# Optimization experiments

Hardware: AMD Instinct MI355X
Metric: run time of the kernel (lower is better)

The kernel has to match this reference:

```python
import jax, jax.numpy as jnp
import numpy as np

N_NODES = 100000


def gcn_conv(x, src, dst, W, b, n):
    # PyG GCNConv: add self-loops, symmetric deg^-1/2 normalization,
    # linear transform, gather->scatter-add aggregation, + bias.
    loop = jnp.arange(n, dtype=src.dtype)
    s = jnp.concatenate([src, loop])
    d = jnp.concatenate([dst, loop])
    deg = jax.ops.segment_sum(jnp.ones_like(d, dtype=x.dtype), d, num_segments=n)
    dinv = jnp.where(deg > 0, jax.lax.rsqrt(deg), jnp.zeros_like(deg))
    norm = dinv[s] * dinv[d]            # [E+N]
    h = x @ W                            # [N, out] (transform before propagate)
    msg = h[s] * norm[:, None]           # gather + scale
    out = jax.ops.segment_sum(msg, d, num_segments=n)  # scatter-add to dst
    return out + b


def setup_inputs() -> dict:
    key = jax.random.key(0)
    k = jax.random.split(key, 6)
    n, e, c_in, hid, c_out = N_NODES, 2500000, 5, 32, 1
    x = jax.random.normal(k[0], (n, c_in), dtype=jnp.float32)
    edge_index = jax.random.randint(k[1], (2, e), 0, n, dtype=jnp.int64)
    # Glorot-style init for GCN weights, zero bias (PyG default)
    W1 = jax.random.normal(k[2], (c_in, hid), dtype=jnp.float32) * (1.0 / np.sqrt(c_in))
    b1 = jnp.zeros((hid,), dtype=jnp.float32)
    W2 = jax.random.normal(k[3], (hid, c_out), dtype=jnp.float32) * (1.0 / np.sqrt(hid))
    b2 = jnp.zeros((c_out,), dtype=jnp.float32)
    return {"x": x, "edge_index": edge_index, "W1": W1, "b1": b1, "W2": W2, "b2": b2}


def reference(x, edge_index, W1, b1, W2, b2):
    n = x.shape[0]
    src, dst = edge_index[0], edge_index[1]
    h = jax.nn.relu(gcn_conv(x, src, dst, W1, b1, n))
    # dropout p=0.3 is identity at inference (training=False)
    return jax.nn.sigmoid(gcn_conv(h, src, dst, W2, b2, n))
```

## Files before the change

kernel.cpp:

```cpp
#include <hip/hip_runtime.h>
#include <math.h>


#define NB_SHIFT  8
#define BNODES    256
#define NBK       512
#define CAP       8192
#define CAP_SHIFT 13
#define CHUNK     4888
#define PBLK      512
#define RPT0      3
#define RPT4      4
#define GBS       16

struct SMemP0 {
    int sp[CHUNK];
    unsigned short sb[CHUNK];
    int cnt[NBK], ofs[NBK], cur[NBK], gbase[NBK];
    int wtmp[8];
};
struct SMemP1 {
    int stage2[CAP];
    int ofs[BNODES], cnt[BNODES], cur[BNODES];
    float w1[160], bb1[32], w2[32];
    int wtmp[8];
};
union SMem { SMemP0 p0; SMemP1 p1; };

__device__ __forceinline__ void gbar_arrive(int* bar, int blk, int tid) {
    __syncthreads();
    if (tid == 0) {
        __threadfence();
        __hip_atomic_fetch_add(&bar[(blk & 7) * GBS], 1, __ATOMIC_RELAXED,
                               __HIP_MEMORY_SCOPE_AGENT);
    }
}
__device__ __forceinline__ void gbar_wait(int* bar, int tgt, int tid) {
    if (tid == 0) {
        for (;;) {
            int s = 0;
#pragma unroll
            for (int k = 0; k < 8; ++k)
                s += __hip_atomic_load(&bar[k * GBS], __ATOMIC_RELAXED,
                                       __HIP_MEMORY_SCOPE_AGENT);
            if (s >= tgt) break;
            __builtin_amdgcn_s_sleep(1);
        }
        __threadfence();
    }
    __syncthreads();
}

__global__ __launch_bounds__(PBLK, 4) void k_fused(
        const int* __restrict__ src, const int* __restrict__ dst, int E,
        const float* __restrict__ x,
        const float* __restrict__ W1, const float* __restrict__ b1,
        const float* __restrict__ W2, const float* __restrict__ b2,
        float* __restrict__ out,
        int* __restrict__ pairs, int* __restrict__ bcur, int* __restrict__ gbar,
        float* __restrict__ h2s, float* __restrict__ xs, int n, int nb) {
    __shared__ SMem sm;
    const int tid  = threadIdx.x;
    const int blk  = blockIdx.x;
    const int G    = gridDim.x;
    const int lane = tid & 63, wv = tid >> 6;
    const int nbase = blk << NB_SHIFT;

    {
        int base = blk * CHUNK;
        if (base < E) {
            int m = min(CHUNK, E - base);
            int m4 = m >> 2;
            int4 dv[RPT0], sv[RPT0];
            int nv = 0;
            const int4* d4 = (const int4*)(dst + base);
            const int4* s4g = (const int4*)(src + base);
#pragma unroll
            for (int j = 0; j < RPT0; ++j) {
                int idx = tid + j * PBLK;
                if (idx < m4) { dv[j] = d4[idx]; sv[j] = s4g[idx]; nv = j + 1; }
            }
            int tb = (m4 << 2) + tid;
            int td = 0, ts = 0, tvalid = 0;
            if (tb < m) { td = dst[base + tb]; ts = src[base + tb]; tvalid = 1; }
            sm.p0.cnt[tid] = 0;
            __syncthreads();
#pragma unroll
            for (int j = 0; j < RPT0; ++j) if (j < nv) {
                atomicAdd(&sm.p0.cnt[dv[j].x >> NB_SHIFT], 1);
                atomicAdd(&sm.p0.cnt[dv[j].y >> NB_SHIFT], 1);
                atomicAdd(&sm.p0.cnt[dv[j].z >> NB_SHIFT], 1);
                atomicAdd(&sm.p0.cnt[dv[j].w >> NB_SHIFT], 1);
            }
            if (tvalid) atomicAdd(&sm.p0.cnt[td >> NB_SHIFT], 1);
            __syncthreads();
            int v = sm.p0.cnt[tid];
            int s = v;
#pragma unroll
            for (int d = 1; d < 64; d <<= 1) {
                int t = __shfl_up(s, d);
                if (lane >= d) s += t;
            }
            if (lane == 63) sm.p0.wtmp[wv] = s;
            __syncthreads();
            if (wv == 0) {
                int t = (lane < 8) ? sm.p0.wtmp[lane] : 0;
#pragma unroll
                for (int d = 1; d < 8; d <<= 1) {
                    int u = __shfl_up(t, d);
                    if (lane >= d) t += u;
                }
                if (lane < 8) sm.p0.wtmp[lane] = t;
            }
            __syncthreads();
            int pre = s + (wv ? sm.p0.wtmp[wv - 1] : 0) - v;
            sm.p0.ofs[tid] = pre;
            sm.p0.cur[tid] = pre;
            sm.p0.gbase[tid] = (tid << CAP_SHIFT)
                             + (v ? atomicAdd(&bcur[tid], v) : 0);
            __syncthreads();
#pragma unroll
            for (int j = 0; j < RPT0; ++j) if (j < nv) {
                int b, p;
                b = dv[j].x >> NB_SHIFT; p = atomicAdd(&sm.p0.cur[b], 1);
                sm.p0.sp[p] = ((dv[j].x & (BNODES - 1)) << 24) | sv[j].x;
                sm.p0.sb[p] = (unsigned short)b;
                b = dv[j].y >> NB_SHIFT; p = atomicAdd(&sm.p0.cur[b], 1);
                sm.p0.sp[p] = ((dv[j].y & (BNODES - 1)) << 24) | sv[j].y;
                sm.p0.sb[p] = (unsigned short)b;
                b = dv[j].z >> NB_SHIFT; p = atomicAdd(&sm.p0.cur[b], 1);
                sm.p0.sp[p] = ((dv[j].z & (BNODES - 1)) << 24) | sv[j].z;
                sm.p0.sb[p] = (unsigned short)b;
                b = dv[j].w >> NB_SHIFT; p = atomicAdd(&sm.p0.cur[b], 1);
                sm.p0.sp[p] = ((dv[j].w & (BNODES - 1)) << 24) | sv[j].w;
                sm.p0.sb[p] = (unsigned short)b;
            }
            if (tvalid) {
                int b = td >> NB_SHIFT;
                int p = atomicAdd(&sm.p0.cur[b], 1);
                sm.p0.sp[p] = ((td & (BNODES - 1)) << 24) | ts;
                sm.p0.sb[p] = (unsigned short)b;
            }
            __syncthreads();
            for (int i = tid; i < m; i += PBLK) {
                int b = sm.p0.sb[i];
                pairs[sm.p0.gbase[b] + (i - sm.p0.ofs[b])] = sm.p0.sp[i];
            }
        }
    }
    gbar_arrive(gbar, blk, tid);
    float xr0 = 0.f, xr1 = 0.f, xr2 = 0.f, xr3 = 0.f, xr4 = 0.f;
    if (blk < nb) {
        if (tid < 160) sm.p1.w1[tid] = W1[tid];
        else if (tid < 192) sm.p1.bb1[tid - 160] = b1[tid - 160];
        else if (tid < 224) sm.p1.w2[tid - 192] = W2[tid - 192];
        if (tid < BNODES) {
            sm.p1.cnt[tid] = 0;
            int node = nbase + tid;
            if (node < n) {
                const float* xp = x + (size_t)node * 5;
                xr0 = xp[0]; xr1 = xp[1]; xr2 = xp[2]; xr3 = xp[3]; xr4 = xp[4];
            }
        }
    }
    gbar_wait(gbar, G, tid);

    int4 rc[RPT4];
    int nv4 = 0, rt = 0, rtv = 0;
    if (blk < nb) {
        int base = blk << CAP_SHIFT;
        int len = min(((volatile int*)bcur)[blk], CAP);
        int len4 = len >> 2;
        const int4* p4 = (const int4*)(pairs + base);
#pragma unroll
        for (int j = 0; j < RPT4; ++j) {
            int idx = tid + j * PBLK;
            if (idx < len4) { rc[j] = p4[idx]; nv4 = j + 1; }
        }
        int i = (len4 << 2) + tid;
        if (i < len) { rt = pairs[base + i]; rtv = 1; }
#pragma unroll
        for (int j = 0; j < RPT4; ++j) if (j < nv4) {
            atomicAdd(&sm.p1.cnt[((unsigned)rc[j].x) >> 24], 1);
            atomicAdd(&sm.p1.cnt[((unsigned)rc[j].y) >> 24], 1);
            atomicAdd(&sm.p1.cnt[((unsigned)rc[j].z) >> 24], 1);
            atomicAdd(&sm.p1.cnt[((unsigned)rc[j].w) >> 24], 1);
        }
        if (rtv) atomicAdd(&sm.p1.cnt[((unsigned)rt) >> 24], 1);
        __syncthreads();
        int v = (tid < BNODES) ? sm.p1.cnt[tid] : 0;
        int s = v;
#pragma unroll
        for (int d = 1; d < 64; d <<= 1) {
            int t = __shfl_up(s, d);
            if (lane >= d) s += t;
        }
        if (lane == 63 && wv < 4) sm.p1.wtmp[wv] = s;
        __syncthreads();
        if (wv == 0) {
            int t = (lane < 4) ? sm.p1.wtmp[lane] : 0;
#pragma unroll
            for (int d = 1; d < 4; d <<= 1) {
                int u = __shfl_up(t, d);
                if (lane >= d) t += u;
            }
            if (lane < 4) sm.p1.wtmp[lane] = t;
        }
        __syncthreads();
        if (tid < BNODES) {
            int pre = s + (wv ? sm.p1.wtmp[wv - 1] : 0) - v;
            sm.p1.ofs[tid] = pre;
            sm.p1.cur[tid] = pre;
            int node = nbase + tid;
            if (node < n) {
                float di = rsqrtf((float)v + 1.0f);
                float* xo = xs + ((size_t)node << 3);
                xo[0] = xr0 * di; xo[1] = xr1 * di; xo[2] = xr2 * di;
                xo[3] = xr3 * di; xo[4] = xr4 * di;
            }
        }
    }
    gbar_arrive(gbar, blk, tid);
    if (blk < nb) {
#pragma unroll
        for (int j = 0; j < RPT4; ++j) if (j < nv4) {
            int p;
            p = atomicAdd(&sm.p1.cur[((unsigned)rc[j].x) >> 24], 1);
            sm.p1.stage2[p] = rc[j].x & 0x00FFFFFF;
            p = atomicAdd(&sm.p1.cur[((unsigned)rc[j].y) >> 24], 1);
            sm.p1.stage2[p] = rc[j].y & 0x00FFFFFF;
            p = atomicAdd(&sm.p1.cur[((unsigned)rc[j].z) >> 24], 1);
            sm.p1.stage2[p] = rc[j].z & 0x00FFFFFF;
            p = atomicAdd(&sm.p1.cur[((unsigned)rc[j].w) >> 24], 1);
            sm.p1.stage2[p] = rc[j].w & 0x00FFFFFF;
        }
        if (rtv) {
            int p = atomicAdd(&sm.p1.cur[((unsigned)rt) >> 24], 1);
            sm.p1.stage2[p] = rt & 0x00FFFFFF;
        }
    }
    gbar_wait(gbar, 2 * G, tid);

    if (blk < nb) {
        int t2 = tid >> 1, half = tid & 1;
        int node = nbase + t2;
        if (node < n) {
            int beg = sm.p1.ofs[t2], dg = sm.p1.cnt[t2];
            float a0 = 0.f, a1 = 0.f, a2 = 0.f, a3 = 0.f, a4 = 0.f;
            if (!half) {
                const float* xo = xs + ((size_t)node << 3);
                a0 = xo[0]; a1 = xo[1]; a2 = xo[2]; a3 = xo[3]; a4 = xo[4];
            }
            for (int e = beg + half; e < beg + dg; e += 2) {
                int sidx = sm.p1.stage2[e];
                const float* xr = xs + ((size_t)sidx << 3);
                float4 q = *(const float4*)xr;
                float q4 = xr[4];
                a0 += q.x; a1 += q.y; a2 += q.z; a3 += q.w; a4 += q4;
            }
            a0 += __shfl_xor(a0, 1); a1 += __shfl_xor(a1, 1);
            a2 += __shfl_xor(a2, 1); a3 += __shfl_xor(a3, 1);
            a4 += __shfl_xor(a4, 1);
            if (!half) {
                float di = rsqrtf((float)dg + 1.0f);
                a0 *= di; a1 *= di; a2 *= di; a3 *= di; a4 *= di;
                float sum = 0.f;
#pragma unroll
                for (int c = 0; c < 32; ++c) {
                    float z = sm.p1.bb1[c] + a0 * sm.p1.w1[c]
                            + a1 * sm.p1.w1[32 + c] + a2 * sm.p1.w1[64 + c]
                            + a3 * sm.p1.w1[96 + c] + a4 * sm.p1.w1[128 + c];
                    sum += fmaxf(z, 0.f) * sm.p1.w2[c];
                }
                h2s[node] = sum * di;
            }
        }
    }
    gbar_arrive(gbar, blk, tid);
    gbar_wait(gbar, 3 * G, tid);

    if (blk < nb) {
        int t2 = tid >> 1, half = tid & 1;
        int node = nbase + t2;
        if (node >= n) return;
        int beg = sm.p1.ofs[t2], dg = sm.p1.cnt[t2];
        float a = 0.f;
        for (int e = beg + half; e < beg + dg; e += 2)
            a += h2s[sm.p1.stage2[e]];
        a += __shfl_xor(a, 1);
        if (!half) {
            float di = rsqrtf((float)dg + 1.0f);
            float vv = di * (a + h2s[node]) + b2[0];
            out[node] = 1.0f / (1.0f + __expf(-vv));
        }
    }
}


__global__ __launch_bounds__(512) void k_part(const int* __restrict__ src,
                                              const int* __restrict__ dst, int E,
                                              int* __restrict__ bcur,
                                              int* __restrict__ pairs) {
    __shared__ int sp[CHUNK];
    __shared__ unsigned short sb[CHUNK];
    __shared__ int cnt[NBK], ofs[NBK], cur[NBK], gbase[NBK];
    int tid = threadIdx.x;
    int base = blockIdx.x * CHUNK;
    int m = min(CHUNK, E - base);

    if (tid < NBK) cnt[tid] = 0;
    __syncthreads();
    for (int i = tid; i < m; i += 2 * 512) {
        int i1 = i + 512;
        int k0 = dst[base + i] >> NB_SHIFT;
        int k1 = (i1 < m) ? (dst[base + i1] >> NB_SHIFT) : -1;
        atomicAdd(&cnt[k0], 1);
        if (k1 >= 0) atomicAdd(&cnt[k1], 1);
    }
    __syncthreads();
    int v = cnt[tid];
    ofs[tid] = v;
    __syncthreads();
    for (int off = 1; off < NBK; off <<= 1) {
        int u = (tid >= off) ? ofs[tid - off] : 0;
        __syncthreads();
        ofs[tid] += u;
        __syncthreads();
    }
    int pre = ofs[tid] - v;
    ofs[tid] = pre;
    cur[tid] = pre;
    gbase[tid] = (tid << CAP_SHIFT) + (v ? atomicAdd(&bcur[tid], v) : 0);
    __syncthreads();
    for (int i = tid; i < m; i += 4 * 512) {
        int ia = i + 512, ib = i + 1024, ic = i + 1536;
        int s0 = src[base + i], d0 = dst[base + i];
        int s1 = 0, d1 = 0, s2 = 0, d2 = 0, s3 = 0, d3 = 0;
        if (ia < m) { s1 = src[base + ia]; d1 = dst[base + ia]; }
        if (ib < m) { s2 = src[base + ib]; d2 = dst[base + ib]; }
        if (ic < m) { s3 = src[base + ic]; d3 = dst[base + ic]; }
        int b0 = d0 >> NB_SHIFT;
        int p0 = atomicAdd(&cur[b0], 1);
        sp[p0] = ((d0 & (BNODES - 1)) << 24) | s0;
        sb[p0] = (unsigned short)b0;
        if (ia < m) {
            int b1 = d1 >> NB_SHIFT;
            int p1 = atomicAdd(&cur[b1], 1);
            sp[p1] = ((d1 & (BNODES - 1)) << 24) | s1;
            sb[p1] = (unsigned short)b1;
        }
        if (ib < m) {
            int b2 = d2 >> NB_SHIFT;
            int p2 = atomicAdd(&cur[b2], 1);
            sp[p2] = ((d2 & (BNODES - 1)) << 24) | s2;
            sb[p2] = (unsigned short)b2;
        }
        if (ic < m) {
            int b3 = d3 >> NB_SHIFT;
            int p3 = atomicAdd(&cur[b3], 1);
            sp[p3] = ((d3 & (BNODES - 1)) << 24) | s3;
            sb[p3] = (unsigned short)b3;
        }
    }
    __syncthreads();
    for (int i = tid; i < m; i += 512) {
        int b = sb[i];
        pairs[gbase[b] + (i - ofs[b])] = sp[i];
    }
}

__global__ __launch_bounds__(512) void k_sorta(const int* __restrict__ pairs,
                                               const int* __restrict__ bcur,
                                               const float* __restrict__ x,
                                               float* __restrict__ dinv,
                                               float* __restrict__ xs,
                                               int* __restrict__ nofs,
                                               int* __restrict__ deg, int n) {
    __shared__ int cnt[BNODES], scn[BNODES];
    int tid = threadIdx.x;
    int b = blockIdx.x;
    int base = b << CAP_SHIFT;
    int len = min(bcur[b], CAP);

    if (tid < BNODES) cnt[tid] = 0;
    __syncthreads();
    for (int i = tid; i < len; i += 512)
        atomicAdd(&cnt[((unsigned)pairs[base + i]) >> 24], 1);
    __syncthreads();
    int v = (tid < BNODES) ? cnt[tid] : 0;
    if (tid < BNODES) scn[tid] = v;
    __syncthreads();
    for (int off = 1; off < BNODES; off <<= 1) {
        int u = (tid < BNODES && tid >= off) ? scn[tid - off] : 0;
        __syncthreads();
        if (tid < BNODES) scn[tid] += u;
        __syncthreads();
    }
    if (tid < BNODES) {
        int node = (b << NB_SHIFT) + tid;
        if (node < n) {
            nofs[node] = base + scn[tid] - v;
            deg[node] = v;
            float di = rsqrtf((float)v + 1.0f);
            dinv[node] = di;
            const float* xr = x + (size_t)node * 5;
            float* xo = xs + ((size_t)node << 3);
#pragma unroll
            for (int k = 0; k < 5; ++k) xo[k] = xr[k] * di;
        }
    }
}

__global__ __launch_bounds__(512) void k_sortagg1(int* __restrict__ pairs,
                                                  const int* __restrict__ bcur,
                                                  const int* __restrict__ nofs,
                                                  const int* __restrict__ deg,
                                                  const float* __restrict__ xs,
                                                  const float* __restrict__ dinv,
                                                  const float* __restrict__ W1,
                                                  const float* __restrict__ b1,
                                                  const float* __restrict__ W2,
                                                  float* __restrict__ h2s, int n) {
    __shared__ int stage2[CAP];
    __shared__ int ofs[BNODES], cnt[BNODES], cur[BNODES];
    __shared__ float w1[160], bb1[32], w2[32];
    int tid = threadIdx.x;
    int b = blockIdx.x;
    int nbase = b << NB_SHIFT;
    int base = b << CAP_SHIFT;
    int len = min(bcur[b], CAP);

    if (tid < 160) w1[tid] = W1[tid];
    else if (tid < 192) bb1[tid - 160] = b1[tid - 160];
    else if (tid < 224) w2[tid - 192] = W2[tid - 192];
    if (tid < BNODES) {
        int node = nbase + tid;
        int o = 0, c = 0;
        if (node < n) { o = nofs[node] - base; c = deg[node]; }
        ofs[tid] = o; cnt[tid] = c; cur[tid] = o;
    }
    __syncthreads();
    for (int i = tid; i < len; i += 2048) {
        int ia = i + 512, ib = i + 1024, ic = i + 1536;
        int v0 = pairs[base + i];
        int v1 = (ia < len) ? pairs[base + ia] : -1;
        int v2 = (ib < len) ? pairs[base + ib] : -1;
        int v3 = (ic < len) ? pairs[base + ic] : -1;
        int p0 = atomicAdd(&cur[((unsigned)v0) >> 24], 1);
        stage2[p0] = v0 & 0x00FFFFFF;
        if (v1 != -1) {
            int p1 = atomicAdd(&cur[((unsigned)v1) >> 24], 1);
            stage2[p1] = v1 & 0x00FFFFFF;
        }
        if (v2 != -1) {
            int p2 = atomicAdd(&cur[((unsigned)v2) >> 24], 1);
            stage2[p2] = v2 & 0x00FFFFFF;
        }
        if (v3 != -1) {
            int p3 = atomicAdd(&cur[((unsigned)v3) >> 24], 1);
            stage2[p3] = v3 & 0x00FFFFFF;
        }
    }
    __syncthreads();
    {
        int len4 = len >> 2;
        const int4* s4 = (const int4*)stage2;
        int4* p4 = (int4*)(pairs + base);
        for (int i = tid; i < len4; i += 512) p4[i] = s4[i];
        for (int i = (len4 << 2) + tid; i < len; i += 512)
            pairs[base + i] = stage2[i];
    }
    int t2 = tid >> 1, half = tid & 1;
    int node = nbase + t2;
    if (node >= n) return;
    int beg = ofs[t2], dg = cnt[t2];
    float a0 = 0.f, a1 = 0.f, a2 = 0.f, a3 = 0.f, a4 = 0.f;
    if (!half) {
        const float* xo = xs + ((size_t)node << 3);
        a0 = xo[0]; a1 = xo[1]; a2 = xo[2]; a3 = xo[3]; a4 = xo[4];
    }
    for (int e = beg + half; e < beg + dg; e += 2) {
        int s = stage2[e];
        const float* xr = xs + ((size_t)s << 3);
        float4 q = *(const float4*)xr;
        float q4 = xr[4];
        a0 += q.x; a1 += q.y; a2 += q.z; a3 += q.w; a4 += q4;
    }
    a0 += __shfl_xor(a0, 1); a1 += __shfl_xor(a1, 1); a2 += __shfl_xor(a2, 1);
    a3 += __shfl_xor(a3, 1); a4 += __shfl_xor(a4, 1);
    if (half) return;
    float di = dinv[node];
    a0 *= di; a1 *= di; a2 *= di; a3 *= di; a4 *= di;
    float sum = 0.f;
#pragma unroll
    for (int c = 0; c < 32; ++c) {
        float z = bb1[c] + a0 * w1[c] + a1 * w1[32 + c] + a2 * w1[64 + c]
                         + a3 * w1[96 + c] + a4 * w1[128 + c];
        sum += fmaxf(z, 0.f) * w2[c];
    }
    h2s[node] = sum * di;
}

__global__ __launch_bounds__(256) void k_agg2(const int* __restrict__ pairs,
                                              const int* __restrict__ nofs,
                                              const int* __restrict__ deg,
                                              const float* __restrict__ h2s,
                                              const float* __restrict__ dinv,
                                              const float* __restrict__ b2,
                                              float* __restrict__ out, int n) {
    int tid = threadIdx.x;
    int node = blockIdx.x * 64 + (tid >> 2);
    int q = tid & 3;
    if (node >= n) return;
    int beg = nofs[node], dg = deg[node];
    float a = 0.f;
    for (int e = beg + q; e < beg + dg; e += 4) a += h2s[pairs[e]];
    a += __shfl_xor(a, 1);
    a += __shfl_xor(a, 2);
    if (q) return;
    float v = dinv[node] * (a + h2s[node]) + b2[0];
    out[node] = 1.0f / (1.0f + __expf(-v));
}

extern "C" void kernel_launch(void* const* d_in, const int* in_sizes, int n_in,
                              void* d_out, int out_size, void* d_ws, size_t ws_size,
                              hipStream_t stream) {
    const float* x  = (const float*)d_in[0];
    const int*   ei = (const int*)d_in[1];
    const float* W1 = (const float*)d_in[2];
    const float* b1 = (const float*)d_in[3];
    const float* W2 = (const float*)d_in[4];
    const float* b2 = (const float*)d_in[5];
    float* out = (float*)d_out;

    const int n = in_sizes[0] / 5;
    const int E = in_sizes[1] / 2;
    const int* src = ei;
    const int* dst = ei + E;
    const int nb = (n + BNODES - 1) >> NB_SHIFT;

    int* wsi = (int*)d_ws;
    int*   pairs = wsi;
    int*   bcur  = wsi + ((size_t)(nb + 1) << CAP_SHIFT);
    int*   gbar  = bcur + NBK;
    int*   deg   = gbar + 8 * GBS;
    int*   nofs  = deg + n;
    float* dinv  = (float*)(nofs + n);
    float* h2s   = dinv + n;
    float* xs    = h2s + n;

    const int nchunk = (E + CHUNK - 1) / CHUNK;
    const int g = nchunk > nb ? nchunk : nb;

    static int use_coop = -1;
    if (use_coop < 0) {
        int dev = 0, ncu = 0, maxb = 0;
        hipGetDevice(&dev);
        hipDeviceGetAttribute(&ncu, hipDeviceAttributeMultiprocessorCount, dev);
        hipError_t e = hipOccupancyMaxActiveBlocksPerMultiprocessor(
                &maxb, k_fused, PBLK, 0);
        int coop = 0;
        hipDeviceGetAttribute(&coop, hipDeviceAttributeCooperativeLaunch, dev);
        use_coop = (e == hipSuccess && coop && (long)maxb * ncu >= g) ? 1 : 0;
    }

    hipMemsetAsync(bcur, 0, (NBK + 8 * GBS) * sizeof(int), stream);

    if (use_coop) {
        void* args[] = {(void*)&src, (void*)&dst, (void*)&E, (void*)&x,
                        (void*)&W1, (void*)&b1, (void*)&W2, (void*)&b2,
                        (void*)&out, (void*)&pairs, (void*)&bcur, (void*)&gbar,
                        (void*)&h2s, (void*)&xs, (void*)&n, (void*)&nb};
        hipError_t e = hipLaunchCooperativeKernel((const void*)k_fused,
                                                  dim3(g), dim3(PBLK),
                                                  args, 0, stream);
        if (e == hipSuccess) return;
        use_coop = 0;
    }

    const int nagg = (n + 63) / 64;
    k_part<<<nchunk, 512, 0, stream>>>(src, dst, E, bcur, pairs);
    k_sorta<<<nb, 512, 0, stream>>>(pairs, bcur, x, dinv, xs, nofs, deg, n);
    k_sortagg1<<<nb, 512, 0, stream>>>(pairs, bcur, nofs, deg, xs, dinv,
                                       W1, b1, W2, h2s, n);
    k_agg2<<<nagg, 256, 0, stream>>>(pairs, nofs, deg, h2s, dinv, b2, out, n);
}
```

Baseline: 141.6 us.

## Halve node-bucket size and edge chunk to double grid in cooperative fused kernel

The cooperative fused kernel now uses 128-node buckets (1024 buckets) and edge chunks of 2444 instead of 256-node buckets and 4888-edge chunks. This roughly doubles the grid and raises occupancy to 8 blocks per CU, with four lanes per node instead of two in the aggregation phases. The aim is better latency hiding and more parallelism across CUs. In exchange the kernel makes more global atomics on bucket counters, and the larger grid adds cost to each grid barrier. If the per-bucket capacity of 4608 is exceeded, edges would be dropped.

Measured after the change: 142.0 us. About the same (+0.3%).

```diff
diff --git a/kernel.cpp b/kernel.cpp
--- a/kernel.cpp
+++ b/kernel.cpp
@@ -1,6 +1,16 @@
 #include <hip/hip_runtime.h>
 #include <math.h>
 
+
+#define PBLK      512
+#define FNB_SHIFT 7
+#define FBNODES   128
+#define FNBK      1024
+#define FCAP      4608
+#define FCHUNK    2444
+#define FRPT0     2
+#define FRPT4     3
+#define GBS       16
 
 #define NB_SHIFT  8
 #define BNODES    256
@@ -8,20 +18,17 @@
 #define CAP       8192
 #define CAP_SHIFT 13
 #define CHUNK     4888
-#define PBLK      512
-#define RPT0      3
-#define RPT4      4
-#define GBS       16
 
 struct SMemP0 {
-    int sp[CHUNK];
-    unsigned short sb[CHUNK];
-    int cnt[NBK], ofs[NBK], cur[NBK], gbase[NBK];
+    int sp[FCHUNK];
+    unsigned short sb[FCHUNK];
+    int cnt[FNBK];
+    int ofs[FNBK], cur[FNBK];
     int wtmp[8];
 };
 struct SMemP1 {
-    int stage2[CAP];
-    int ofs[BNODES], cnt[BNODES], cur[BNODES];
+    int stage2[FCAP];
+    int ofs[FBNODES], cnt[FBNODES], cur[FBNODES];
     float w1[160], bb1[32], w2[32];
     int wtmp[8];
 };
@@ -51,32 +58,32 @@
     __syncthreads();
 }
 
-__global__ __launch_bounds__(PBLK, 4) void k_fused(
+__global__ __launch_bounds__(PBLK, 8) void k_fused(
         const int* __restrict__ src, const int* __restrict__ dst, int E,
         const float* __restrict__ x,
         const float* __restrict__ W1, const float* __restrict__ b1,
         const float* __restrict__ W2, const float* __restrict__ b2,
         float* __restrict__ out,
         int* __restrict__ pairs, int* __restrict__ bcur, int* __restrict__ gbar,
-        float* __restrict__ h2s, float* __restrict__ xs, int n, int nb) {
+        float* __restrict__ h2s, float* __restrict__ xs, int n, int fnb) {
     __shared__ SMem sm;
     const int tid  = threadIdx.x;
     const int blk  = blockIdx.x;
     const int G    = gridDim.x;
     const int lane = tid & 63, wv = tid >> 6;
-    const int nbase = blk << NB_SHIFT;
+    const int nbase = blk << FNB_SHIFT;
 
     {
-        int base = blk * CHUNK;
+        int base = blk * FCHUNK;
         if (base < E) {
-            int m = min(CHUNK, E - base);
+            int m = min(FCHUNK, E - base);
             int m4 = m >> 2;
-            int4 dv[RPT0], sv[RPT0];
+            int4 dv[FRPT0], sv[FRPT0];
             int nv = 0;
-            const int4* d4 = (const int4*)(dst + base);
+            const int4* d4  = (const int4*)(dst + base);
             const int4* s4g = (const int4*)(src + base);
 #pragma unroll
-            for (int j = 0; j < RPT0; ++j) {
+            for (int j = 0; j < FRPT0; ++j) {
                 int idx = tid + j * PBLK;
                 if (idx < m4) { dv[j] = d4[idx]; sv[j] = s4g[idx]; nv = j + 1; }
             }
@@ -84,18 +91,21 @@
             int td = 0, ts = 0, tvalid = 0;
             if (tb < m) { td = dst[base + tb]; ts = src[base + tb]; tvalid = 1; }
             sm.p0.cnt[tid] = 0;
+            sm.p0.cnt[tid + PBLK] = 0;
             __syncthreads();
 #pragma unroll
-            for (int j = 0; j < RPT0; ++j) if (j < nv) {
-                atomicAdd(&sm.p0.cnt[dv[j].x >> NB_SHIFT], 1);
-                atomicAdd(&sm.p0.cnt[dv[j].y >> NB_SHIFT], 1);
-                atomicAdd(&sm.p0.cnt[dv[j].z >> NB_SHIFT], 1);
-                atomicAdd(&sm.p0.cnt[dv[j].w >> NB_SHIFT], 1);
-            }
-            if (tvalid) atomicAdd(&sm.p0.cnt[td >> NB_SHIFT], 1);
+            for (int j = 0; j < FRPT0; ++j) if (j < nv) {
+                atomicAdd(&sm.p0.cnt[dv[j].x >> FNB_SHIFT], 1);
+                atomicAdd(&sm.p0.cnt[dv[j].y >> FNB_SHIFT], 1);
+                atomicAdd(&sm.p0.cnt[dv[j].z >> FNB_SHIFT], 1);
+                atomicAdd(&sm.p0.cnt[dv[j].w >> FNB_SHIFT], 1);
+            }
+            if (tvalid) atomicAdd(&sm.p0.cnt[td >> FNB_SHIFT], 1);
             __syncthreads();
-            int v = sm.p0.cnt[tid];
-            int s = v;
+            int v0 = sm.p0.cnt[2 * tid];
+            int v1 = sm.p0.cnt[2 * tid + 1];
+            int loc = v0 + v1;
+            int s = loc;
 #pragma unroll
             for (int d = 1; d < 64; d <<= 1) {
                 int t = __shfl_up(s, d);
@@ -113,48 +123,50 @@
                 if (lane < 8) sm.p0.wtmp[lane] = t;
             }
             __syncthreads();
-            int pre = s + (wv ? sm.p0.wtmp[wv - 1] : 0) - v;
-            sm.p0.ofs[tid] = pre;
-            sm.p0.cur[tid] = pre;
-            sm.p0.gbase[tid] = (tid << CAP_SHIFT)
-                             + (v ? atomicAdd(&bcur[tid], v) : 0);
+            int pre = s - loc + (wv ? sm.p0.wtmp[wv - 1] : 0);
+            sm.p0.ofs[2 * tid] = pre;         sm.p0.cur[2 * tid] = pre;
+            sm.p0.ofs[2 * tid + 1] = pre + v0; sm.p0.cur[2 * tid + 1] = pre + v0;
+            sm.p0.cnt[2 * tid] = 2 * tid * FCAP
+                               + (v0 ? atomicAdd(&bcur[2 * tid], v0) : 0);
+            sm.p0.cnt[2 * tid + 1] = (2 * tid + 1) * FCAP
+                               + (v1 ? atomicAdd(&bcur[2 * tid + 1], v1) : 0);
             __syncthreads();
 #pragma unroll
-            for (int j = 0; j < RPT0; ++j) if (j < nv) {
+            for (int j = 0; j < FRPT0; ++j) if (j < nv) {
                 int b, p;
-                b = dv[j].x >> NB_SHIFT; p = atomicAdd(&sm.p0.cur[b], 1);
-                sm.p0.sp[p] = ((dv[j].x & (BNODES - 1)) << 24) | sv[j].x;
+                b = dv[j].x >> FNB_SHIFT; p = atomicAdd(&sm.p0.cur[b], 1);
+                sm.p0.sp[p] = ((dv[j].x & (FBNODES - 1)) << 24) | sv[j].x;
                 sm.p0.sb[p] = (unsigned short)b;
-                b = dv[j].y >> NB_SHIFT; p = atomicAdd(&sm.p0.cur[b], 1);
-                sm.p0.sp[p] = ((dv[j].y & (BNODES - 1)) << 24) | sv[j].y;
+                b = dv[j].y >> FNB_SHIFT; p = atomicAdd(&sm.p0.cur[b], 1);
+                sm.p0.sp[p] = ((dv[j].y & (FBNODES - 1)) << 24) | sv[j].y;
                 sm.p0.sb[p] = (unsigned short)b;
-                b = dv[j].z >> NB_SHIFT; p = atomicAdd(&sm.p0.cur[b], 1);
-                sm.p0.sp[p] = ((dv[j].z & (BNODES - 1)) << 24) | sv[j].z;
+                b = dv[j].z >> FNB_SHIFT; p = atomicAdd(&sm.p0.cur[b], 1);
+                sm.p0.sp[p] = ((dv[j].z & (FBNODES - 1)) << 24) | sv[j].z;
                 sm.p0.sb[p] = (unsigned short)b;
-                b = dv[j].w >> NB_SHIFT; p = atomicAdd(&sm.p0.cur[b], 1);
-                sm.p0.sp[p] = ((dv[j].w & (BNODES - 1)) << 24) | sv[j].w;
+                b = dv[j].w >> FNB_SHIFT; p = atomicAdd(&sm.p0.cur[b], 1);
+                sm.p0.sp[p] = ((dv[j].w & (FBNODES - 1)) << 24) | sv[j].w;
                 sm.p0.sb[p] = (unsigned short)b;
             }
             if (tvalid) {
-                int b = td >> NB_SHIFT;
+                int b = td >> FNB_SHIFT;
                 int p = atomicAdd(&sm.p0.cur[b], 1);
-                sm.p0.sp[p] = ((td & (BNODES - 1)) << 24) | ts;
+                sm.p0.sp[p] = ((td & (FBNODES - 1)) << 24) | ts;
                 sm.p0.sb[p] = (unsigned short)b;
             }
             __syncthreads();
             for (int i = tid; i < m; i += PBLK) {
                 int b = sm.p0.sb[i];
-                pairs[sm.p0.gbase[b] + (i - sm.p0.ofs[b])] = sm.p0.sp[i];
+                pairs[sm.p0.cnt[b] + (i - sm.p0.ofs[b])] = sm.p0.sp[i];
             }
         }
     }
     gbar_arrive(gbar, blk, tid);
     float xr0 = 0.f, xr1 = 0.f, xr2 = 0.f, xr3 = 0.f, xr4 = 0.f;
-    if (blk < nb) {
+    if (blk < fnb) {
         if (tid < 160) sm.p1.w1[tid] = W1[tid];
         else if (tid < 192) sm.p1.bb1[tid - 160] = b1[tid - 160];
         else if (tid < 224) sm.p1.w2[tid - 192] = W2[tid - 192];
-        if (tid < BNODES) {
+        if (tid < FBNODES) {
             sm.p1.cnt[tid] = 0;
             int node = nbase + tid;
             if (node < n) {
@@ -165,22 +177,22 @@
     }
     gbar_wait(gbar, G, tid);
 
-    int4 rc[RPT4];
+    int4 rc[FRPT4];
     int nv4 = 0, rt = 0, rtv = 0;
-    if (blk < nb) {
-        int base = blk << CAP_SHIFT;
-        int len = min(((volatile int*)bcur)[blk], CAP);
+    if (blk < fnb) {
+        int pbase = blk * FCAP;
+        int len = min(((volatile int*)bcur)[blk], FCAP);
         int len4 = len >> 2;
-        const int4* p4 = (const int4*)(pairs + base);
-#pragma unroll
-        for (int j = 0; j < RPT4; ++j) {
+        const int4* p4 = (const int4*)(pairs + pbase);
+#pragma unroll
+        for (int j = 0; j < FRPT4; ++j) {
             int idx = tid + j * PBLK;
             if (idx < len4) { rc[j] = p4[idx]; nv4 = j + 1; }
         }
         int i = (len4 << 2) + tid;
-        if (i < len) { rt = pairs[base + i]; rtv = 1; }
-#pragma unroll
-        for (int j = 0; j < RPT4; ++j) if (j < nv4) {
+        if (i < len) { rt = pairs[pbase + i]; rtv = 1; }
+#pragma unroll
+        for (int j = 0; j < FRPT4; ++j) if (j < nv4) {
             atomicAdd(&sm.p1.cnt[((unsigned)rc[j].x) >> 24], 1);
             atomicAdd(&sm.p1.cnt[((unsigned)rc[j].y) >> 24], 1);
             atomicAdd(&sm.p1.cnt[((unsigned)rc[j].z) >> 24], 1);
@@ -188,26 +200,23 @@
         }
         if (rtv) atomicAdd(&sm.p1.cnt[((unsigned)rt) >> 24], 1);
         __syncthreads();
-        int v = (tid < BNODES) ? sm.p1.cnt[tid] : 0;
+        int v = (tid < FBNODES) ? sm.p1.cnt[tid] : 0;
         int s = v;
 #pragma unroll
         for (int d = 1; d < 64; d <<= 1) {
             int t = __shfl_up(s, d);
             if (lane >= d) s += t;
         }
-        if (lane == 63 && wv < 4) sm.p1.wtmp[wv] = s;
+        if (lane == 63 && wv < 2) sm.p1.wtmp[wv] = s;
         __syncthreads();
         if (wv == 0) {
-            int t = (lane < 4) ? sm.p1.wtmp[lane] : 0;
-#pragma unroll
-            for (int d = 1; d < 4; d <<= 1) {
-                int u = __shfl_up(t, d);
-                if (lane >= d) t += u;
-            }
-            if (lane < 4) sm.p1.wtmp[lane] = t;
+            int t = (lane < 2) ? sm.p1.wtmp[lane] : 0;
+            int u = __shfl_up(t, 1);
+            if (lane >= 1) t += u;
+            if (lane < 2) sm.p1.wtmp[lane] = t;
         }
         __syncthreads();
-        if (tid < BNODES) {
+        if (tid < FBNODES) {
             int pre = s + (wv ? sm.p1.wtmp[wv - 1] : 0) - v;
             sm.p1.ofs[tid] = pre;
             sm.p1.cur[tid] = pre;
@@ -221,9 +230,9 @@
         }
     }
     gbar_arrive(gbar, blk, tid);
-    if (blk < nb) {
-#pragma unroll
-        for (int j = 0; j < RPT4; ++j) if (j < nv4) {
+    if (blk < fnb) {
+#pragma unroll
+        for (int j = 0; j < FRPT4; ++j) if (j < nv4) {
             int p;
             p = atomicAdd(&sm.p1.cur[((unsigned)rc[j].x) >> 24], 1);
             sm.p1.stage2[p] = rc[j].x & 0x00FFFFFF;
@@ -241,27 +250,29 @@
     }
     gbar_wait(gbar, 2 * G, tid);
 
-    if (blk < nb) {
-        int t2 = tid >> 1, half = tid & 1;
-        int node = nbase + t2;
+    if (blk < fnb) {
+        int t4 = tid >> 2, q = tid & 3;
+        int node = nbase + t4;
         if (node < n) {
-            int beg = sm.p1.ofs[t2], dg = sm.p1.cnt[t2];
+            int beg = sm.p1.ofs[t4], dg = sm.p1.cnt[t4];
             float a0 = 0.f, a1 = 0.f, a2 = 0.f, a3 = 0.f, a4 = 0.f;
-            if (!half) {
+            if (q == 0) {
                 const float* xo = xs + ((size_t)node << 3);
                 a0 = xo[0]; a1 = xo[1]; a2 = xo[2]; a3 = xo[3]; a4 = xo[4];
             }
-            for (int e = beg + half; e < beg + dg; e += 2) {
+            for (int e = beg + q; e < beg + dg; e += 4) {
                 int sidx = sm.p1.stage2[e];
                 const float* xr = xs + ((size_t)sidx << 3);
-                float4 q = *(const float4*)xr;
+                float4 qv = *(const float4*)xr;
                 float q4 = xr[4];
-                a0 += q.x; a1 += q.y; a2 += q.z; a3 += q.w; a4 += q4;
-            }
-            a0 += __shfl_xor(a0, 1); a1 += __shfl_xor(a1, 1);
-            a2 += __shfl_xor(a2, 1); a3 += __shfl_xor(a3, 1);
-            a4 += __shfl_xor(a4, 1);
-            if (!half) {
+                a0 += qv.x; a1 += qv.y; a2 += qv.z; a3 += qv.w; a4 += q4;
+            }
+            a0 += __shfl_xor(a0, 1); a0 += __shfl_xor(a0, 2);
+            a1 += __shfl_xor(a1, 1); a1 += __shfl_xor(a1, 2);
+            a2 += __shfl_xor(a2, 1); a2 += __shfl_xor(a2, 2);
+            a3 += __shfl_xor(a3, 1); a3 += __shfl_xor(a3, 2);
+            a4 += __shfl_xor(a4, 1); a4 += __shfl_xor(a4, 2);
+            if (q == 0) {
                 float di = rsqrtf((float)dg + 1.0f);
                 a0 *= di; a1 *= di; a2 *= di; a3 *= di; a4 *= di;
                 float sum = 0.f;
@@ -279,16 +290,17 @@
     gbar_arrive(gbar, blk, tid);
     gbar_wait(gbar, 3 * G, tid);
 
-    if (blk < nb) {
-        int t2 = tid >> 1, half = tid & 1;
-        int node = nbase + t2;
+    if (blk < fnb) {
+        int t4 = tid >> 2, q = tid & 3;
+        int node = nbase + t4;
         if (node >= n) return;
-        int beg = sm.p1.ofs[t2], dg = sm.p1.cnt[t2];
+        int beg = sm.p1.ofs[t4], dg = sm.p1.cnt[t4];
         float a = 0.f;
-        for (int e = beg + half; e < beg + dg; e += 2)
+        for (int e = beg + q; e < beg + dg; e += 4)
             a += h2s[sm.p1.stage2[e]];
         a += __shfl_xor(a, 1);
-        if (!half) {
+        a += __shfl_xor(a, 2);
+        if (q == 0) {
             float di = rsqrtf((float)dg + 1.0f);
             float vv = di * (a + h2s[node]) + b2[0];
             out[node] = 1.0f / (1.0f + __expf(-vv));
@@ -537,20 +549,17 @@
     const int E = in_sizes[1] / 2;
     const int* src = ei;
     const int* dst = ei + E;
-    const int nb = (n + BNODES - 1) >> NB_SHIFT;
 
     int* wsi = (int*)d_ws;
-    int*   pairs = wsi;
-    int*   bcur  = wsi + ((size_t)(nb + 1) << CAP_SHIFT);
-    int*   gbar  = bcur + NBK;
-    int*   deg   = gbar + 8 * GBS;
-    int*   nofs  = deg + n;
-    float* dinv  = (float*)(nofs + n);
-    float* h2s   = dinv + n;
-    float* xs    = h2s + n;
-
-    const int nchunk = (E + CHUNK - 1) / CHUNK;
-    const int g = nchunk > nb ? nchunk : nb;
+
+    const int fnb    = (n + FBNODES - 1) >> FNB_SHIFT;
+    const int fchnk  = (E + FCHUNK - 1) / FCHUNK;
+    const int g      = fchnk > fnb ? fchnk : fnb;
+    int*   fpairs = wsi;
+    int*   fbcur  = wsi + (size_t)FNBK * FCAP;
+    int*   fgbar  = fbcur + FNBK;
+    float* fh2s   = (float*)(fgbar + 8 * GBS);
+    float* fxs    = fh2s + n;
 
     static int use_coop = -1;
     if (use_coop < 0) {
@@ -564,13 +573,13 @@
         use_coop = (e == hipSuccess && coop && (long)maxb * ncu >= g) ? 1 : 0;
     }
 
-    hipMemsetAsync(bcur, 0, (NBK + 8 * GBS) * sizeof(int), stream);
-
     if (use_coop) {
+        hipMemsetAsync(fbcur, 0, (FNBK + 8 * GBS) * sizeof(int), stream);
         void* args[] = {(void*)&src, (void*)&dst, (void*)&E, (void*)&x,
                         (void*)&W1, (void*)&b1, (void*)&W2, (void*)&b2,
-                        (void*)&out, (void*)&pairs, (void*)&bcur, (void*)&gbar,
-                        (void*)&h2s, (void*)&xs, (void*)&n, (void*)&nb};
+                        (void*)&out, (void*)&fpairs, (void*)&fbcur,
+                        (void*)&fgbar, (void*)&fh2s, (void*)&fxs,
+                        (void*)&n, (void*)&fnb};
         hipError_t e = hipLaunchCooperativeKernel((const void*)k_fused,
                                                   dim3(g), dim3(PBLK),
                                                   args, 0, stream);
@@ -578,7 +587,18 @@
         use_coop = 0;
     }
 
-    const int nagg = (n + 63) / 64;
+    const int nb = (n + BNODES - 1) >> NB_SHIFT;
+    int*   pairs = wsi;
+    int*   bcur  = wsi + ((size_t)(nb + 1) << CAP_SHIFT);
+    int*   deg   = bcur + NBK;
+    int*   nofs  = deg + n;
+    float* dinv  = (float*)(nofs + n);
+    float* h2s   = dinv + n;
+    float* xs    = h2s + n;
+    const int nchunk = (E + CHUNK - 1) / CHUNK;
+    const int nagg   = (n + 63) / 64;
+
+    hipMemsetAsync(bcur, 0, NBK * sizeof(int), stream);
     k_part<<<nchunk, 512, 0, stream>>>(src, dst, E, bcur, pairs);
     k_sorta<<<nb, 512, 0, stream>>>(pairs, bcur, x, dinv, xs, nofs, deg, n);
     k_sortagg1<<<nb, 512, 0, stream>>>(pairs, bcur, nofs, deg, xs, dinv,
```
